# Performance work log

Measured on AMD Instinct MI355X. Metric: run time of the kernel, lower is better.

The kernel has to match this reference:

```python
import jax, jax.numpy as jnp
import numpy as np

B, S, H = 2, 256, 256
R = H  # rdim defaults to hidden_size


def setup_inputs() -> dict:
    key = jax.random.key(0)
    k1, k2, k3 = jax.random.split(key, 3)
    hidden_states = jax.random.normal(k1, (B, S, H), dtype=jnp.float32)
    # Linear weights stored torch-style [out, in]
    Wqkv = jax.random.normal(k2, (3 * R, H), dtype=jnp.float32) * (H ** -0.5)
    bqkv = jnp.zeros((3 * R,), dtype=jnp.float32)
    Wc = jax.random.normal(k3, (R, R), dtype=jnp.float32) * (R ** -0.5)
    bc = jnp.zeros((R,), dtype=jnp.float32)
    return {"hidden_states": hidden_states, "Wqkv": Wqkv, "bqkv": bqkv, "Wc": Wc, "bc": bc}


def reference(hidden_states, Wqkv, bqkv, Wc, bc):
    # qkv projection: [B,S,3R]
    qkv = jnp.einsum('bsh,rh->bsr', hidden_states, Wqkv) + bqkv
    q, k, v = jnp.split(qkv, 3, axis=-1)  # each [B,S,R]
    # Tucker-style outer-product scores: [B,S,L,R]
    scores = jnp.einsum('bsr,blr->bslr', q, k)
    # c_proj mixes the r dimension
    scores = jnp.einsum('bslr,pr->bslp', scores, Wc) + bc
    # rearrange 'b s l r -> (b r) s l' + softmax(dim=-1) == softmax over l axis
    probs = jax.nn.softmax(scores, axis=2)
    # 'brsl,blr->bsr' after rearrange back == 'bslr,blr->bsr'
    return jnp.einsum('bslr,blr->bsr', probs, v)
```

## Files before the change

### kernel.cpp

```cpp
#include <hip/hip_runtime.h>
#include <hip/hip_bf16.h>
#include <math.h>

typedef __bf16 bf16;
typedef _Float16 f16;
typedef __attribute__((ext_vector_type(8))) __bf16 bf16x8;
typedef __attribute__((ext_vector_type(8))) _Float16 f16x8;
typedef __attribute__((ext_vector_type(4))) _Float16 f16x4;
typedef __attribute__((ext_vector_type(4))) float floatx4;

__device__ __forceinline__ void split8(floatx4 a0, floatx4 a1, bf16x8& hi, bf16x8& lo) {
#pragma unroll
    for (int t = 0; t < 4; t++) {
        float v0 = a0[t], v1 = a1[t];
        bf16 h0 = (bf16)v0, h1 = (bf16)v1;
        hi[t] = h0;     lo[t] = (bf16)(v0 - (float)h0);
        hi[t + 4] = h1; lo[t + 4] = (bf16)(v1 - (float)h1);
    }
}

__global__ __launch_bounds__(256, 4)
void proj_kernel(const float* __restrict__ hs, const float* __restrict__ Wq,
                 const float* __restrict__ bq, const float* __restrict__ Wc,
                 f16* __restrict__ q_ws, f16* __restrict__ k_ws,
                 f16* __restrict__ vT_ws, f16* __restrict__ Wc_ws)
{
    const int tid = threadIdx.x;
    if (blockIdx.x >= 384) {
        const int base = (blockIdx.x - 384) * 1024 + tid * 4;
        floatx4 w = *(const floatx4*)(Wc + base);
        f16x4 h;
        h.x = (f16)w.x; h.y = (f16)w.y; h.z = (f16)w.z; h.w = (f16)w.w;
        *(f16x4*)(Wc_ws + base) = h;
        return;
    }
    const int wv = tid >> 6, lane = tid & 63;
    const int quad = lane >> 4, lcol = lane & 15;
    const int wt = blockIdx.x * 4 + wv;
    const int rt = wt / 48, ct = wt - rt * 48;
    const int row0 = rt * 16, col0 = ct * 16;

    const float* arow = hs + (row0 + lcol) * 256;
    const float* brow = Wq + (col0 + lcol) * 256;

    floatx4 acc = {0.f, 0.f, 0.f, 0.f};
#pragma unroll
    for (int ks = 0; ks < 8; ks++) {
        const int h = ks * 32 + quad * 8;
        floatx4 a0 = *(const floatx4*)(arow + h);
        floatx4 a1 = *(const floatx4*)(arow + h + 4);
        floatx4 b0 = *(const floatx4*)(brow + h);
        floatx4 b1 = *(const floatx4*)(brow + h + 4);
        bf16x8 ahi, alo, bhi, blo;
        split8(a0, a1, ahi, alo);
        split8(b0, b1, bhi, blo);
        acc = __builtin_amdgcn_mfma_f32_16x16x32_bf16(ahi, bhi, acc, 0, 0, 0);
        acc = __builtin_amdgcn_mfma_f32_16x16x32_bf16(ahi, blo, acc, 0, 0, 0);
        acc = __builtin_amdgcn_mfma_f32_16x16x32_bf16(alo, bhi, acc, 0, 0, 0);
    }
    const float bias = bq[col0 + lcol];
    const int col = col0 + lcol, seg = col0 >> 8, jj = col & 255;
#pragma unroll
    for (int r = 0; r < 4; r++) {
        const int row = row0 + quad * 4 + r;
        const float val = acc[r] + bias;
        if (seg == 0)      q_ws[row * 256 + jj] = (f16)val;
        else if (seg == 1) k_ws[row * 256 + jj] = (f16)val;
        else               vT_ws[(row >> 8) * 65536 + jj * 256 + (row & 255)] = (f16)val;
    }
}

__global__ __launch_bounds__(512, 2)
void attn_partial(const f16* __restrict__ qw, const f16* __restrict__ kw,
                  const f16* __restrict__ vT, const f16* __restrict__ Wc16,
                  float* __restrict__ osum_ws, float* __restrict__ ssum_ws)
{
    __shared__ f16 Klds[64 * 256];
    __shared__ f16 Wlds[64 * 256];
    __shared__ f16 vTlds[64 * 68];

    const int bid = blockIdx.x;
    const int pt = bid & 3;
    const int lq = (bid >> 2) & 3;
    const int sg = (bid >> 4) & 31;
    const int b  = bid >> 9;
    const int p0 = pt * 64;
    const int l0 = lq * 64;
    const int tid  = threadIdx.x;
    const int wv   = tid >> 6;
    const int lane = tid & 63;
    const int quad = lane >> 4, lcol = lane & 15;
    const int ph = wv & 1, sp = wv >> 1;
    const int s_base = sg * 8 + sp * 2;

    const f16* kbase = kw + b * 65536;
    const f16* vbase = vT + b * 65536;
    const f16* qbase = qw + (b * 256 + s_base) * 256;

#pragma unroll
    for (int it = 0; it < 4; it++) {
        const int id = it * 512 + tid;
        const int r = id >> 5, c = id & 31;
        const int csrc = c ^ (r & 7);
        *(uint4*)(Klds + r * 256 + c * 8) =
            *(const uint4*)(kbase + (l0 + r) * 256 + csrc * 8);
    }
#pragma unroll
    for (int it = 0; it < 4; it++) {
        const int id = it * 512 + tid;
        const int r = id >> 5, c = id & 31;
        const int csrc = c ^ (r & 7);
        *(uint4*)(Wlds + r * 256 + c * 8) =
            *(const uint4*)(Wc16 + (p0 + r) * 256 + csrc * 8);
    }
#pragma unroll
    for (int it = 0; it < 2; it++) {
        const int id = it * 512 + tid;
        const int p = id >> 4, c = id & 15;
        *(f16x4*)(vTlds + p * 68 + c * 4) =
            *(const f16x4*)(vbase + (p0 + p) * 256 + l0 + c * 4);
    }
    __syncthreads();

    floatx4 acc[2][4][2];
#pragma unroll
    for (int u = 0; u < 2; u++)
#pragma unroll
        for (int i = 0; i < 4; i++)
#pragma unroll
            for (int j = 0; j < 2; j++)
                acc[u][i][j] = (floatx4){0.f, 0.f, 0.f, 0.f};

#pragma unroll
    for (int kk = 0; kk < 8; kk++) {
        const int rb = kk * 32 + quad * 8;
        const int sw = ((kk * 4 + quad) ^ (lcol & 7)) << 3;
        f16x8 qv0 = *(const f16x8*)(qbase + rb);
        f16x8 qv1 = *(const f16x8*)(qbase + 256 + rb);
        f16x8 kf[4];
#pragma unroll
        for (int i = 0; i < 4; i++)
            kf[i] = *(const f16x8*)(Klds + (i * 16 + lcol) * 256 + sw);
        f16x8 w8[2];
#pragma unroll
        for (int j = 0; j < 2; j++)
            w8[j] = *(const f16x8*)(Wlds + (ph * 32 + j * 16 + lcol) * 256 + sw);
#pragma unroll
        for (int j = 0; j < 2; j++) {
            f16x8 bf0 = w8[j] * qv0;
            f16x8 bf1 = w8[j] * qv1;
#pragma unroll
            for (int i = 0; i < 4; i++) {
                acc[0][i][j] = __builtin_amdgcn_mfma_f32_16x16x32_f16(kf[i], bf0, acc[0][i][j], 0, 0, 0);
                acc[1][i][j] = __builtin_amdgcn_mfma_f32_16x16x32_f16(kf[i], bf1, acc[1][i][j], 0, 0, 0);
            }
        }
    }

    float os[2][2] = {{0.f,0.f},{0.f,0.f}};
    float ss[2][2] = {{0.f,0.f},{0.f,0.f}};
#pragma unroll
    for (int i = 0; i < 4; i++) {
#pragma unroll
        for (int j = 0; j < 2; j++) {
            f16x4 vf = *(const f16x4*)(vTlds + (ph * 32 + j * 16 + lcol) * 68 + i * 16 + quad * 4);
            const float vF0 = (float)vf[0], vF1 = (float)vf[1], vF2 = (float)vf[2], vF3 = (float)vf[3];
#pragma unroll
            for (int u = 0; u < 2; u++) {
                const float P0 = __expf(acc[u][i][j][0]);
                const float P1 = __expf(acc[u][i][j][1]);
                const float P2 = __expf(acc[u][i][j][2]);
                const float P3 = __expf(acc[u][i][j][3]);
                os[u][j] = fmaf(P0, vF0, os[u][j]);
                os[u][j] = fmaf(P1, vF1, os[u][j]);
                os[u][j] = fmaf(P2, vF2, os[u][j]);
                os[u][j] = fmaf(P3, vF3, os[u][j]);
                ss[u][j] += (P0 + P1) + (P2 + P3);
            }
        }
    }

#pragma unroll
    for (int u = 0; u < 2; u++)
#pragma unroll
        for (int j = 0; j < 2; j++) {
            os[u][j] += __shfl_xor(os[u][j], 16);
            os[u][j] += __shfl_xor(os[u][j], 32);
            ss[u][j] += __shfl_xor(ss[u][j], 16);
            ss[u][j] += __shfl_xor(ss[u][j], 32);
        }
    if (quad == 0) {
#pragma unroll
        for (int u = 0; u < 2; u++) {
            const int base = ((b * 256 + s_base + u) * 4 + lq) * 256 + p0 + ph * 32;
#pragma unroll
            for (int j = 0; j < 2; j++) {
                osum_ws[base + j * 16 + lcol] = os[u][j];
                ssum_ws[base + j * 16 + lcol] = ss[u][j];
            }
        }
    }
}

__global__ __launch_bounds__(256, 4)
void merge_kernel(const float* __restrict__ osum_ws, const float* __restrict__ ssum_ws,
                  float* __restrict__ out)
{
    const int g = blockIdx.x * 256 + threadIdx.x;
    const int p = g & 255, bs = g >> 8;
    const int base = bs * 1024 + p;
    float O = 0.f, S = 0.f;
#pragma unroll
    for (int lq = 0; lq < 4; lq++) {
        O += osum_ws[base + lq * 256];
        S += ssum_ws[base + lq * 256];
    }
    out[g] = O / S;
}

extern "C" void kernel_launch(void* const* d_in, const int* in_sizes, int n_in,
                              void* d_out, int out_size, void* d_ws, size_t ws_size,
                              hipStream_t stream) {
    const float* hs   = (const float*)d_in[0];
    const float* Wqkv = (const float*)d_in[1];
    const float* bqkv = (const float*)d_in[2];
    const float* Wc   = (const float*)d_in[3];
    float* out = (float*)d_out;

    char* ws = (char*)d_ws;
    f16* q_ws   = (f16*)ws;
    f16* k_ws   = (f16*)(ws + 262144);
    f16* vT_ws  = (f16*)(ws + 524288);
    f16* Wc_ws  = (f16*)(ws + 786432);
    float* osum_ws = (float*)(ws + 1048576);
    float* ssum_ws = (float*)(ws + 3145728);

    proj_kernel<<<dim3(448), 256, 0, stream>>>(hs, Wqkv, bqkv, Wc, q_ws, k_ws, vT_ws, Wc_ws);
    attn_partial<<<dim3(1024), 512, 0, stream>>>(q_ws, k_ws, vT_ws, Wc_ws, osum_ws, ssum_ws);
    merge_kernel<<<dim3(512), 256, 0, stream>>>(osum_ws, ssum_ws, out);
}
```

Measured before the change: 90.42 us.

## Fuse merge into attention kernel via last-block atomic counter

Removes the separate merge kernel launch. Each attention block writes its partial sums, fences, and bumps a per-(b, s-group, p-tile) atomic counter. The last of the four l-quarter blocks reduces the partials and writes the output. The counters are zeroed in the projection kernel. This saves one launch and its gap, at the cost of extra fences and a serialized tail of work in the last-arriving blocks.

```diff
diff --git a/kernel.cpp b/kernel.cpp
--- a/kernel.cpp
+++ b/kernel.cpp
@@ -23,10 +23,12 @@
 void proj_kernel(const float* __restrict__ hs, const float* __restrict__ Wq,
                  const float* __restrict__ bq, const float* __restrict__ Wc,
                  f16* __restrict__ q_ws, f16* __restrict__ k_ws,
-                 f16* __restrict__ vT_ws, f16* __restrict__ Wc_ws)
+                 f16* __restrict__ vT_ws, f16* __restrict__ Wc_ws,
+                 int* __restrict__ cnt)
 {
     const int tid = threadIdx.x;
     if (blockIdx.x >= 384) {
+        if (blockIdx.x == 384) cnt[tid] = 0;
         const int base = (blockIdx.x - 384) * 1024 + tid * 4;
         floatx4 w = *(const floatx4*)(Wc + base);
         f16x4 h;
@@ -73,11 +75,13 @@
 __global__ __launch_bounds__(512, 2)
 void attn_partial(const f16* __restrict__ qw, const f16* __restrict__ kw,
                   const f16* __restrict__ vT, const f16* __restrict__ Wc16,
-                  float* __restrict__ osum_ws, float* __restrict__ ssum_ws)
+                  float* __restrict__ osum_ws, float* __restrict__ ssum_ws,
+                  int* __restrict__ cnt, float* __restrict__ out)
 {
     __shared__ f16 Klds[64 * 256];
     __shared__ f16 Wlds[64 * 256];
     __shared__ f16 vTlds[64 * 68];
+    __shared__ int last_flag;
 
     const int bid = blockIdx.x;
     const int pt = bid & 3;
@@ -200,22 +204,23 @@
             }
         }
     }
-}
-
-__global__ __launch_bounds__(256, 4)
-void merge_kernel(const float* __restrict__ osum_ws, const float* __restrict__ ssum_ws,
-                  float* __restrict__ out)
-{
-    const int g = blockIdx.x * 256 + threadIdx.x;
-    const int p = g & 255, bs = g >> 8;
-    const int base = bs * 1024 + p;
-    float O = 0.f, S = 0.f;
-#pragma unroll
-    for (int lq = 0; lq < 4; lq++) {
-        O += osum_ws[base + lq * 256];
-        S += ssum_ws[base + lq * 256];
-    }
-    out[g] = O / S;
+
+    __threadfence();
+    __syncthreads();
+    if (tid == 0) {
+        const int cidx = (b * 32 + sg) * 4 + pt;
+        last_flag = (atomicAdd(&cnt[cidx], 1) == 3);
+    }
+    __syncthreads();
+    if (last_flag) {
+        __threadfence();
+        const int s  = sg * 8 + (tid >> 6);
+        const int pp = tid & 63;
+        const int base = (b * 256 + s) * 1024 + p0 + pp;
+        const float O = osum_ws[base] + osum_ws[base + 256] + osum_ws[base + 512] + osum_ws[base + 768];
+        const float S = ssum_ws[base] + ssum_ws[base + 256] + ssum_ws[base + 512] + ssum_ws[base + 768];
+        out[(b * 256 + s) * 256 + p0 + pp] = O / S;
+    }
 }
 
 extern "C" void kernel_launch(void* const* d_in, const int* in_sizes, int n_in,
@@ -234,8 +239,8 @@
     f16* Wc_ws  = (f16*)(ws + 786432);
     float* osum_ws = (float*)(ws + 1048576);
     float* ssum_ws = (float*)(ws + 3145728);
-
-    proj_kernel<<<dim3(448), 256, 0, stream>>>(hs, Wqkv, bqkv, Wc, q_ws, k_ws, vT_ws, Wc_ws);
-    attn_partial<<<dim3(1024), 512, 0, stream>>>(q_ws, k_ws, vT_ws, Wc_ws, osum_ws, ssum_ws);
-    merge_kernel<<<dim3(512), 256, 0, stream>>>(osum_ws, ssum_ws, out);
-}
+    int*   cnt_ws  = (int*)(ws + 5242880);
+
+    proj_kernel<<<dim3(448), 256, 0, stream>>>(hs, Wqkv, bqkv, Wc, q_ws, k_ws, vT_ws, Wc_ws, cnt_ws);
+    attn_partial<<<dim3(1024), 512, 0, stream>>>(q_ws, k_ws, vT_ws, Wc_ws, osum_ws, ssum_ws, cnt_ws, out);
+}
```

Measured after the change: 296.6 us. 3.28x slower.
